# Optimization experiments

Measured on AMD Instinct MI355X. Metric: run time of the kernel, lower is better.

The kernel has to match this reference:

```python
import jax, jax.numpy as jnp
import numpy as np

D_MODEL = 1024
NUM_HEADS = 16
HEAD_DIM = D_MODEL // NUM_HEADS
D_FF = 4 * D_MODEL


def setup_inputs() -> dict:
    key = jax.random.key(0)
    ks = jax.random.split(key, 16)
    s = 0.02
    inp = {
        "x": jax.random.normal(ks[0], (2, 2048, D_MODEL), dtype=jnp.float32),
        "w_q": jax.random.normal(ks[1], (D_MODEL, D_MODEL), dtype=jnp.float32) * s,
        "b_q": jnp.zeros((D_MODEL,), jnp.float32),
        "w_k": jax.random.normal(ks[2], (D_MODEL, D_MODEL), dtype=jnp.float32) * s,
        "b_k": jnp.zeros((D_MODEL,), jnp.float32),
        "w_v": jax.random.normal(ks[3], (D_MODEL, D_MODEL), dtype=jnp.float32) * s,
        "b_v": jnp.zeros((D_MODEL,), jnp.float32),
        "w_o": jax.random.normal(ks[4], (D_MODEL, D_MODEL), dtype=jnp.float32) * s,
        "b_o": jnp.zeros((D_MODEL,), jnp.float32),
        "w_ff1": jax.random.normal(ks[5], (D_MODEL, D_FF), dtype=jnp.float32) * s,
        "b_ff1": jnp.zeros((D_FF,), jnp.float32),
        "w_ff2": jax.random.normal(ks[6], (D_FF, D_MODEL), dtype=jnp.float32) * s,
        "b_ff2": jnp.zeros((D_MODEL,), jnp.float32),
        "ln1_g": jnp.ones((D_MODEL,), jnp.float32),
        "ln1_b": jnp.zeros((D_MODEL,), jnp.float32),
        "ln2_g": jnp.ones((D_MODEL,), jnp.float32),
        "ln2_b": jnp.zeros((D_MODEL,), jnp.float32),
    }
    return inp


def layer_norm(x, g, b, eps=1e-5):
    mu = jnp.mean(x, axis=-1, keepdims=True)
    var = jnp.var(x, axis=-1, keepdims=True)
    return (x - mu) * jax.lax.rsqrt(var + eps) * g + b


def encoder_block(x, w_q, b_q, w_k, b_k, w_v, b_v, w_o, b_o,
                  w_ff1, b_ff1, w_ff2, b_ff2, ln1_g, ln1_b, ln2_g, ln2_b):
    B, S, _ = x.shape
    # QKV projections -> [B, H, S, hd]
    def proj(w, b):
        return (x @ w + b).reshape(B, S, NUM_HEADS, HEAD_DIM).transpose(0, 2, 1, 3)
    q, k, v = proj(w_q, b_q), proj(w_k, b_k), proj(w_v, b_v)
    scale = 1.0 / jnp.sqrt(jnp.float32(HEAD_DIM))
    score = jnp.einsum('bhqd,bhkd->bhqk', q, k) * scale  # [B,H,S,S]
    attn = jax.nn.softmax(score, axis=-1)
    ctx = jnp.einsum('bhqk,bhkd->bhqd', attn, v)
    ctx = ctx.transpose(0, 2, 1, 3).reshape(B, S, D_MODEL)
    attn_out = ctx @ w_o + b_o
    # AddNorm1 (dropout = identity at inference)
    h = layer_norm(x + attn_out, ln1_g, ln1_b)
    # FFN
    ff = jax.nn.relu(h @ w_ff1 + b_ff1) @ w_ff2 + b_ff2
    # AddNorm2
    return layer_norm(h + ff, ln2_g, ln2_b)


def reference(x, w_q, b_q, w_k, b_k, w_v, b_v, w_o, b_o,
              w_ff1, b_ff1, w_ff2, b_ff2, ln1_g, ln1_b, ln2_g, ln2_b):
    return encoder_block(x, w_q, b_q, w_k, b_k, w_v, b_v, w_o, b_o,
                         w_ff1, b_ff1, w_ff2, b_ff2, ln1_g, ln1_b, ln2_g, ln2_b)
```

## Files before the change

kernel.cpp:

```cpp
#include <hip/hip_runtime.h>
#include <hip/hip_bf16.h>

typedef __attribute__((ext_vector_type(8))) short short8;
typedef __attribute__((ext_vector_type(4))) float f32x4;
typedef unsigned short u16;
typedef unsigned int u32;

constexpr float CSC = 0.18033688f;

__device__ __forceinline__ u16 f2bf(float f) {
    __hip_bfloat16 h = __float2bfloat16(f);
    return __builtin_bit_cast(u16, h);
}
__device__ __forceinline__ u32 packtrunc(float a, float b) {
    const u32 ua = __builtin_bit_cast(u32, a);
    const u32 ub = __builtin_bit_cast(u32, b);
    return (ua >> 16) | (ub & 0xffff0000u);
}

#if __has_builtin(__builtin_amdgcn_exp2f)
#define EXP2(x) __builtin_amdgcn_exp2f(x)
#else
#define EXP2(x) exp2f(x)
#endif

#define GLD16(g, l) __builtin_amdgcn_global_load_lds( \
    (const __attribute__((address_space(1))) void*)(g), \
    (__attribute__((address_space(3))) void*)(l), 16, 0, 0)

__global__ __launch_bounds__(256) void prep_kernel(
    const float* __restrict__ x, u16* __restrict__ xb,
    const float* __restrict__ w_q, const float* __restrict__ w_k,
    const float* __restrict__ w_v, const float* __restrict__ w_o,
    const float* __restrict__ w_ff1, const float* __restrict__ w_ff2,
    u16* __restrict__ wqkvT, u16* __restrict__ woT,
    u16* __restrict__ wf1T, u16* __restrict__ wf2T,
    const float* __restrict__ bq, const float* __restrict__ bk,
    const float* __restrict__ bv, float* __restrict__ bout)
{
    __shared__ float tile[32][33];
    int id = blockIdx.x;
    const int t = threadIdx.x;
    if (id < 1024) {
        const int i = id * 256 + t;
        float4 v = ((const float4*)x)[i];
        *(ushort4*)(xb + 4 * (size_t)i) =
            make_ushort4(f2bf(v.x), f2bf(v.y), f2bf(v.z), f2bf(v.w));
        return;
    }
    id -= 1024;
    const float* src; u16* dst; int R, C, bx, by;
    if (id < 4096) {
        const int w = id >> 10, tt = id & 1023;
        src = w == 0 ? w_q : (w == 1 ? w_k : (w == 2 ? w_v : w_o));
        dst = w < 3 ? wqkvT + (size_t)w * 1024 * 1024 : woT;
        R = 1024; C = 1024; bx = (tt & 31) * 32; by = (tt >> 5) * 32;
    } else if (id < 8192) {
        const int tt = id - 4096;
        src = w_ff1; dst = wf1T;
        R = 1024; C = 4096; bx = (tt & 127) * 32; by = (tt >> 7) * 32;
    } else if (id < 12288) {
        const int tt = id - 8192;
        src = w_ff2; dst = wf2T;
        R = 4096; C = 1024; bx = (tt & 31) * 32; by = (tt >> 5) * 32;
    } else {
        for (int i = t; i < 1024; i += 256) {
            bout[i] = bq[i]; bout[1024 + i] = bk[i]; bout[2048 + i] = bv[i];
        }
        return;
    }
    const int tx = t & 31, ty = t >> 5;
    #pragma unroll
    for (int i = 0; i < 32; i += 8)
        tile[ty + i][tx] = src[(size_t)(by + ty + i) * C + bx + tx];
    __syncthreads();
    #pragma unroll
    for (int i = 0; i < 32; i += 8)
        dst[(size_t)(bx + ty + i) * R + by + tx] = f2bf(tile[tx][ty + i]);
}

template<bool RELU, int TM, bool QKV>
__global__ __launch_bounds__(256, 3) void gemm_bt(
    const u16* __restrict__ A, const u16* __restrict__ BT,
    const float* __restrict__ bias, u16* __restrict__ C,
    u16* __restrict__ VT, int M, int N, int K)
{
    __shared__ __align__(16) u16 As[TM * 32];
    __shared__ __align__(16) u16 Bs[128 * 32];
    constexpr int MW = TM / 32;
    constexpr int NCH_A = TM * 4;
    constexpr int NITER = (NCH_A + 512) / 256;
    const int t = threadIdx.x;
    const int wave = t >> 6, lane = t & 63;
    const int quad = lane >> 4, l16 = lane & 15;
    const int wm = (wave >> 1) * (TM / 2), wn = (wave & 1) * 64;
    const size_t rowA = (size_t)blockIdx.x * TM;
    const size_t rowB = (size_t)blockIdx.y * 128;

    f32x4 acc[MW][4] = {};

    for (int k0 = 0; k0 < K; k0 += 32) {
        __syncthreads();
        #pragma unroll
        for (int j = 0; j < NITER; ++j) {
            const int cb = j * 256 + wave * 64;
            const int c = cb + lane;
            if (j * 256 < NCH_A) {
                const int m = c >> 2, kq = c & 3;
                GLD16(A + (rowA + m) * K + k0 + kq * 8, As + cb * 8);
            } else {
                const int c2 = c - NCH_A;
                const int m = c2 >> 2, kq = c2 & 3;
                GLD16(BT + (rowB + m) * K + k0 + kq * 8, Bs + (cb - NCH_A) * 8);
            }
        }
        __syncthreads();
        short8 af[MW], bf[4];
        #pragma unroll
        for (int i = 0; i < MW; ++i)
            af[i] = *(const short8*)(As + (wm + i * 16 + l16) * 32 + quad * 8);
        #pragma unroll
        for (int j = 0; j < 4; ++j)
            bf[j] = *(const short8*)(Bs + (wn + j * 16 + l16) * 32 + quad * 8);
        #pragma unroll
        for (int i = 0; i < MW; ++i)
            #pragma unroll
            for (int j = 0; j < 4; ++j)
                acc[i][j] = __builtin_amdgcn_mfma_f32_16x16x32_bf16(
                    af[i], bf[j], acc[i][j], 0, 0, 0);
    }

    if (QKV && (int)blockIdx.y >= 16) {
        #pragma unroll
        for (int i = 0; i < MW; ++i) {
            #pragma unroll
            for (int j = 0; j < 4; ++j) {
                const int vcol = (int)rowB + wn + j * 16 + l16 - 2048;
                const int hh = vcol >> 6, dd = vcol & 63;
                const float bv = bias[vcol + 2048];
                const int row0 = (int)rowA + wm + i * 16 + quad * 4;
                const int bb = row0 >> 11, ss = row0 & 2047;
                ushort4 pk;
                pk.x = f2bf(acc[i][j][0] + bv);
                pk.y = f2bf(acc[i][j][1] + bv);
                pk.z = f2bf(acc[i][j][2] + bv);
                pk.w = f2bf(acc[i][j][3] + bv);
                *(ushort4*)(VT + ((size_t)(bb * 16 + hh) * 64 + dd) * 2048 + ss) = pk;
            }
        }
    } else {
        const float sc = (QKV && (int)blockIdx.y < 8) ? CSC : 1.0f;
        #pragma unroll
        for (int i = 0; i < MW; ++i) {
            #pragma unroll
            for (int j = 0; j < 4; ++j) {
                const int col = (int)rowB + wn + j * 16 + l16;
                const float bv = bias[col];
                #pragma unroll
                for (int r = 0; r < 4; ++r) {
                    const int row = (int)rowA + wm + i * 16 + quad * 4 + r;
                    float v = (acc[i][j][r] + bv) * sc;
                    if (RELU) v = fmaxf(v, 0.f);
                    C[(size_t)row * N + col] = f2bf(v);
                }
            }
        }
    }
}

template<int TM>
__global__ __launch_bounds__(256, 3) void gemm_bt_sk(
    const u16* __restrict__ A, const u16* __restrict__ BT,
    float* __restrict__ Cp0, float* __restrict__ Cp1,
    int M, int N, int K, int Kspl)
{
    __shared__ __align__(16) u16 As[TM * 32];
    __shared__ __align__(16) u16 Bs[128 * 32];
    constexpr int MW = TM / 32;
    constexpr int NCH_A = TM * 4;
    constexpr int NITER = (NCH_A + 512) / 256;
    const int t = threadIdx.x;
    const int wave = t >> 6, lane = t & 63;
    const int quad = lane >> 4, l16 = lane & 15;
    const int wm = (wave >> 1) * (TM / 2), wn = (wave & 1) * 64;
    const size_t rowA = (size_t)blockIdx.x * TM;
    const size_t rowB = (size_t)blockIdx.y * 128;
    const int kbeg = blockIdx.z * Kspl;

    f32x4 acc[MW][4] = {};

    for (int k0 = kbeg; k0 < kbeg + Kspl; k0 += 32) {
        __syncthreads();
        #pragma unroll
        for (int j = 0; j < NITER; ++j) {
            const int cb = j * 256 + wave * 64;
            const int c = cb + lane;
            if (j * 256 < NCH_A) {
                const int m = c >> 2, kq = c & 3;
                GLD16(A + (rowA + m) * K + k0 + kq * 8, As + cb * 8);
            } else {
                const int c2 = c - NCH_A;
                const int m = c2 >> 2, kq = c2 & 3;
                GLD16(BT + (rowB + m) * K + k0 + kq * 8, Bs + (cb - NCH_A) * 8);
            }
        }
        __syncthreads();
        short8 af[MW], bf[4];
        #pragma unroll
        for (int i = 0; i < MW; ++i)
            af[i] = *(const short8*)(As + (wm + i * 16 + l16) * 32 + quad * 8);
        #pragma unroll
        for (int j = 0; j < 4; ++j)
            bf[j] = *(const short8*)(Bs + (wn + j * 16 + l16) * 32 + quad * 8);
        #pragma unroll
        for (int i = 0; i < MW; ++i)
            #pragma unroll
            for (int j = 0; j < 4; ++j)
                acc[i][j] = __builtin_amdgcn_mfma_f32_16x16x32_bf16(
                    af[i], bf[j], acc[i][j], 0, 0, 0);
    }

    float* out = blockIdx.z == 0 ? Cp0 : Cp1;
    #pragma unroll
    for (int i = 0; i < MW; ++i)
        #pragma unroll
        for (int j = 0; j < 4; ++j) {
            const int col = (int)rowB + wn + j * 16 + l16;
            #pragma unroll
            for (int r = 0; r < 4; ++r) {
                const int row = (int)rowA + wm + i * 16 + quad * 4 + r;
                out[(size_t)row * N + col] = acc[i][j][r];
            }
        }
}

__global__ __launch_bounds__(256, 2) void flash_attn(
    const u16* __restrict__ qkv, const u16* __restrict__ vt,
    u16* __restrict__ ctx)
{
    __shared__ __align__(16) u16 Ks[64 * 64];
    __shared__ __align__(16) u16 Vs[64 * 64];
    __shared__ __align__(16) u16 Ps[4 * 32 * 72];
    const int t = threadIdx.x;
    const int wave = t >> 6, lane = t & 63;
    const int quad = lane >> 4, l16 = lane & 15;
    const int h = blockIdx.y, b = blockIdx.z;
    const int q0 = blockIdx.x * 128 + wave * 32;
    const size_t rowbase = (size_t)b * 2048;
    const u16* kb = qkv + rowbase * 3072 + 1024 + h * 64;
    const u16* vb = vt + (size_t)(b * 16 + h) * 64 * 2048;
    u16* pw = Ps + wave * 32 * 72;

    short8 aq[2][2];
    #pragma unroll
    for (int m2 = 0; m2 < 2; ++m2)
        #pragma unroll
        for (int ksb = 0; ksb < 2; ++ksb)
            aq[m2][ksb] = *(const short8*)(qkv +
                (rowbase + q0 + m2 * 16 + l16) * 3072 + h * 64 + ksb * 32 + quad * 8);

    f32x4 o[2][4] = {};
    f32x4 lp4[2] = {};

    for (int kv0 = 0; kv0 < 2048; kv0 += 64) {
        __syncthreads();
        #pragma unroll
        for (int j = 0; j < 2; ++j) {
            const int cb = j * 256 + wave * 64;
            const int slot = cb + lane;
            const int row = slot >> 3;
            const int kq = (slot & 7) ^ (row & 7);
            GLD16(kb + (size_t)(kv0 + row) * 3072 + kq * 8, Ks + cb * 8);
            GLD16(vb + (size_t)row * 2048 + kv0 + kq * 8, Vs + cb * 8);
        }
        __syncthreads();

        f32x4 st[2][4] = {};
        #pragma unroll
        for (int ksb = 0; ksb < 2; ++ksb) {
            short8 ak[4];
            #pragma unroll
            for (int mt = 0; mt < 4; ++mt)
                ak[mt] = *(const short8*)(Ks +
                    ((mt * 16 + l16) * 8 + ((ksb * 4 + quad) ^ (l16 & 7))) * 8);
            #pragma unroll
            for (int m2 = 0; m2 < 2; ++m2)
                #pragma unroll
                for (int mt = 0; mt < 4; ++mt)
                    st[m2][mt] = __builtin_amdgcn_mfma_f32_16x16x32_bf16(
                        ak[mt], aq[m2][ksb], st[m2][mt], 0, 0, 0);
        }

        #pragma unroll
        for (int m2 = 0; m2 < 2; ++m2) {
            #pragma unroll
            for (int mt = 0; mt < 4; ++mt) {
                const float p0 = EXP2(st[m2][mt][0]);
                const float p1 = EXP2(st[m2][mt][1]);
                const float p2 = EXP2(st[m2][mt][2]);
                const float p3 = EXP2(st[m2][mt][3]);
                lp4[m2] = lp4[m2] + (f32x4){p0, p1, p2, p3};
                *(uint2*)(pw + (m2 * 16 + l16) * 72 + mt * 16 + quad * 4) =
                    make_uint2(packtrunc(p0, p1), packtrunc(p2, p3));
            }
        }

        #pragma unroll
        for (int ksb = 0; ksb < 2; ++ksb) {
            short8 bv[4];
            #pragma unroll
            for (int dt = 0; dt < 4; ++dt)
                bv[dt] = *(const short8*)(Vs +
                    ((dt * 16 + l16) * 8 + ((ksb * 4 + quad) ^ (l16 & 7))) * 8);
            #pragma unroll
            for (int m2 = 0; m2 < 2; ++m2) {
                const short8 ap = *(const short8*)(pw +
                    (m2 * 16 + l16) * 72 + ksb * 32 + quad * 8);
                #pragma unroll
                for (int dt = 0; dt < 4; ++dt)
                    o[m2][dt] = __builtin_amdgcn_mfma_f32_16x16x32_bf16(
                        ap, bv[dt], o[m2][dt], 0, 0, 0);
            }
        }
    }

    #pragma unroll
    for (int m2 = 0; m2 < 2; ++m2) {
        float lp = (lp4[m2][0] + lp4[m2][1]) + (lp4[m2][2] + lp4[m2][3]);
        lp += __shfl_xor(lp, 16, 64);
        lp += __shfl_xor(lp, 32, 64);
        #pragma unroll
        for (int r = 0; r < 4; ++r) {
            const float inv = 1.0f / __shfl(lp, quad * 4 + r, 64);
            const size_t row = rowbase + q0 + m2 * 16 + quad * 4 + r;
            #pragma unroll
            for (int dt = 0; dt < 4; ++dt)
                ctx[row * 1024 + h * 64 + dt * 16 + l16] = f2bf(o[m2][dt][r] * inv);
        }
    }
}

__global__ __launch_bounds__(256) void add_norm_p_kernel(
    const float* __restrict__ a, const float* __restrict__ p0,
    const float* __restrict__ p1, const float* __restrict__ cb,
    const float* __restrict__ g, const float* __restrict__ bbv,
    float* __restrict__ out32, u16* __restrict__ out16)
{
    __shared__ float red[8];
    const int row = blockIdx.x, t = threadIdx.x;
    const int wave = t >> 6, lane = t & 63;
    const size_t base = (size_t)row * 1024 + t * 4;
    const int c = t * 4;
    float4 av = *(const float4*)(a + base);
    float4 q0 = *(const float4*)(p0 + base);
    float4 q1 = *(const float4*)(p1 + base);
    float4 cv = *(const float4*)(cb + c);
    float v0 = av.x + q0.x + q1.x + cv.x;
    float v1 = av.y + q0.y + q1.y + cv.y;
    float v2 = av.z + q0.z + q1.z + cv.z;
    float v3 = av.w + q0.w + q1.w + cv.w;
    float sum = v0 + v1 + v2 + v3;
    float sq  = v0 * v0 + v1 * v1 + v2 * v2 + v3 * v3;
    #pragma unroll
    for (int msk = 1; msk < 64; msk <<= 1) {
        sum += __shfl_xor(sum, msk, 64);
        sq  += __shfl_xor(sq,  msk, 64);
    }
    if (lane == 0) { red[wave] = sum; red[wave + 4] = sq; }
    __syncthreads();
    sum = red[0] + red[1] + red[2] + red[3];
    sq  = red[4] + red[5] + red[6] + red[7];
    const float mu  = sum * (1.f / 1024.f);
    const float var = sq * (1.f / 1024.f) - mu * mu;
    const float rstd = rsqrtf(var + 1e-5f);
    float o0 = (v0 - mu) * rstd * g[c + 0] + bbv[c + 0];
    float o1 = (v1 - mu) * rstd * g[c + 1] + bbv[c + 1];
    float o2 = (v2 - mu) * rstd * g[c + 2] + bbv[c + 2];
    float o3 = (v3 - mu) * rstd * g[c + 3] + bbv[c + 3];
    *(float4*)(out32 + base) = make_float4(o0, o1, o2, o3);
    if (out16)
        *(ushort4*)(out16 + base) = make_ushort4(f2bf(o0), f2bf(o1), f2bf(o2), f2bf(o3));
}

extern "C" void kernel_launch(void* const* d_in, const int* in_sizes, int n_in,
                              void* d_out, int out_size, void* d_ws, size_t ws_size,
                              hipStream_t stream)
{
    const float* x     = (const float*)d_in[0];
    const float* w_q   = (const float*)d_in[1];
    const float* b_q   = (const float*)d_in[2];
    const float* w_k   = (const float*)d_in[3];
    const float* b_k   = (const float*)d_in[4];
    const float* w_v   = (const float*)d_in[5];
    const float* b_v   = (const float*)d_in[6];
    const float* w_o   = (const float*)d_in[7];
    const float* b_o   = (const float*)d_in[8];
    const float* w_ff1 = (const float*)d_in[9];
    const float* b_ff1 = (const float*)d_in[10];
    const float* w_ff2 = (const float*)d_in[11];
    const float* b_ff2 = (const float*)d_in[12];
    const float* ln1_g = (const float*)d_in[13];
    const float* ln1_b = (const float*)d_in[14];
    const float* ln2_g = (const float*)d_in[15];
    const float* ln2_b = (const float*)d_in[16];

    char* ws = (char*)d_ws;
    u16*   xb    = (u16*)(ws);
    u16*   wqkvT = (u16*)(ws + (8ull  << 20));
    u16*   woT   = (u16*)(ws + (14ull << 20));
    u16*   wf1T  = (u16*)(ws + (16ull << 20));
    u16*   wf2T  = (u16*)(ws + (24ull << 20));
    float* bqkv  = (float*)(ws + (32ull << 20));
    u16*   qkv   = (u16*)(ws + (33ull << 20));
    u16*   ctx   = (u16*)(ws + (57ull << 20));
    float* h32   = (float*)(ws + (65ull << 20));
    u16*   hb    = (u16*)(ws + (81ull << 20));
    u16*   ff    = (u16*)(ws + (89ull << 20));
    u16*   vt    = (u16*)(ws + (121ull << 20));
    float* pO0   = (float*)(ws + (33ull << 20));
    float* pO1   = (float*)(ws + (121ull << 20));
    float* pF0   = (float*)(ws + (33ull << 20));
    float* pF1   = (float*)(ws + (49ull << 20));

    prep_kernel<<<13313, 256, 0, stream>>>(
        x, xb, w_q, w_k, w_v, w_o, w_ff1, w_ff2,
        wqkvT, woT, wf1T, wf2T, b_q, b_k, b_v, bqkv);

    gemm_bt<false, 128, true ><<<dim3(32, 24), 256, 0, stream>>>(
        xb, wqkvT, bqkv, qkv, vt, 4096, 3072, 1024);
    flash_attn<<<dim3(16, 16, 2), 256, 0, stream>>>(qkv, vt, ctx);
    gemm_bt_sk<128><<<dim3(32, 8, 2), 256, 0, stream>>>(
        ctx, woT, pO0, pO1, 4096, 1024, 1024, 512);
    add_norm_p_kernel<<<4096, 256, 0, stream>>>(
        x, pO0, pO1, b_o, ln1_g, ln1_b, h32, hb);
    gemm_bt<true, 128, false><<<dim3(32, 32), 256, 0, stream>>>(
        hb, wf1T, b_ff1, ff, nullptr, 4096, 4096, 1024);
    gemm_bt_sk<128><<<dim3(32, 8, 2), 256, 0, stream>>>(
        ff, wf2T, pF0, pF1, 4096, 1024, 4096, 2048);
    add_norm_p_kernel<<<4096, 256, 0, stream>>>(
        h32, pF0, pF1, b_ff2, ln2_g, ln2_b, (float*)d_out, nullptr);
}
```

Baseline: 349.2 us.

## Store split-K partials as bf16 and shrink split-K GEMM tiles to 64 rows

The split-K GEMMs for the output projection and FFN2 now write their partial sums as bf16 instead of fp32, and the add-norm kernel reads and converts them, halving partial-buffer traffic. The split-K tile height drops from 128 to 64 with twice the grid in M, and launch bounds ask for 4 blocks per CU, for more parallelism. Rounding each partial to bf16 before the residual add loses accuracy, and the smaller tiles reduce operand reuse.

After: 345.9 us. No clear change (-0.9%).

```diff
diff --git a/kernel.cpp b/kernel.cpp
--- a/kernel.cpp
+++ b/kernel.cpp
@@ -11,6 +11,10 @@
 __device__ __forceinline__ u16 f2bf(float f) {
     __hip_bfloat16 h = __float2bfloat16(f);
     return __builtin_bit_cast(u16, h);
+}
+__device__ __forceinline__ float bf2f(u16 u) {
+    __hip_bfloat16 h = __builtin_bit_cast(__hip_bfloat16, u);
+    return __bfloat162float(h);
 }
 __device__ __forceinline__ u32 packtrunc(float a, float b) {
     const u32 ua = __builtin_bit_cast(u32, a);
@@ -169,9 +173,9 @@
 }
 
 template<int TM>
-__global__ __launch_bounds__(256, 3) void gemm_bt_sk(
+__global__ __launch_bounds__(256, 4) void gemm_bt_sk(
     const u16* __restrict__ A, const u16* __restrict__ BT,
-    float* __restrict__ Cp0, float* __restrict__ Cp1,
+    u16* __restrict__ Cp0, u16* __restrict__ Cp1,
     int M, int N, int K, int Kspl)
 {
     __shared__ __align__(16) u16 As[TM * 32];
@@ -220,7 +224,7 @@
                     af[i], bf[j], acc[i][j], 0, 0, 0);
     }
 
-    float* out = blockIdx.z == 0 ? Cp0 : Cp1;
+    u16* out = blockIdx.z == 0 ? Cp0 : Cp1;
     #pragma unroll
     for (int i = 0; i < MW; ++i)
         #pragma unroll
@@ -229,7 +233,7 @@
             #pragma unroll
             for (int r = 0; r < 4; ++r) {
                 const int row = (int)rowA + wm + i * 16 + quad * 4 + r;
-                out[(size_t)row * N + col] = acc[i][j][r];
+                out[(size_t)row * N + col] = f2bf(acc[i][j][r]);
             }
         }
 }
@@ -341,8 +345,8 @@
 }
 
 __global__ __launch_bounds__(256) void add_norm_p_kernel(
-    const float* __restrict__ a, const float* __restrict__ p0,
-    const float* __restrict__ p1, const float* __restrict__ cb,
+    const float* __restrict__ a, const u16* __restrict__ p0,
+    const u16* __restrict__ p1, const float* __restrict__ cb,
     const float* __restrict__ g, const float* __restrict__ bbv,
     float* __restrict__ out32, u16* __restrict__ out16)
 {
@@ -352,13 +356,13 @@
     const size_t base = (size_t)row * 1024 + t * 4;
     const int c = t * 4;
     float4 av = *(const float4*)(a + base);
-    float4 q0 = *(const float4*)(p0 + base);
-    float4 q1 = *(const float4*)(p1 + base);
+    ushort4 u0 = *(const ushort4*)(p0 + base);
+    ushort4 u1 = *(const ushort4*)(p1 + base);
     float4 cv = *(const float4*)(cb + c);
-    float v0 = av.x + q0.x + q1.x + cv.x;
-    float v1 = av.y + q0.y + q1.y + cv.y;
-    float v2 = av.z + q0.z + q1.z + cv.z;
-    float v3 = av.w + q0.w + q1.w + cv.w;
+    float v0 = av.x + bf2f(u0.x) + bf2f(u1.x) + cv.x;
+    float v1 = av.y + bf2f(u0.y) + bf2f(u1.y) + cv.y;
+    float v2 = av.z + bf2f(u0.z) + bf2f(u1.z) + cv.z;
+    float v3 = av.w + bf2f(u0.w) + bf2f(u1.w) + cv.w;
     float sum = v0 + v1 + v2 + v3;
     float sq  = v0 * v0 + v1 * v1 + v2 * v2 + v3 * v3;
     #pragma unroll
@@ -417,10 +421,10 @@
     u16*   hb    = (u16*)(ws + (81ull << 20));
     u16*   ff    = (u16*)(ws + (89ull << 20));
     u16*   vt    = (u16*)(ws + (121ull << 20));
-    float* pO0   = (float*)(ws + (33ull << 20));
-    float* pO1   = (float*)(ws + (121ull << 20));
-    float* pF0   = (float*)(ws + (33ull << 20));
-    float* pF1   = (float*)(ws + (49ull << 20));
+    u16*   pO0   = (u16*)(ws + (33ull << 20));
+    u16*   pO1   = (u16*)(ws + (41ull << 20));
+    u16*   pF0   = (u16*)(ws + (33ull << 20));
+    u16*   pF1   = (u16*)(ws + (41ull << 20));
 
     prep_kernel<<<13313, 256, 0, stream>>>(
         x, xb, w_q, w_k, w_v, w_o, w_ff1, w_ff2,
@@ -429,13 +433,13 @@
     gemm_bt<false, 128, true ><<<dim3(32, 24), 256, 0, stream>>>(
         xb, wqkvT, bqkv, qkv, vt, 4096, 3072, 1024);
     flash_attn<<<dim3(16, 16, 2), 256, 0, stream>>>(qkv, vt, ctx);
-    gemm_bt_sk<128><<<dim3(32, 8, 2), 256, 0, stream>>>(
+    gemm_bt_sk<64><<<dim3(64, 8, 2), 256, 0, stream>>>(
         ctx, woT, pO0, pO1, 4096, 1024, 1024, 512);
     add_norm_p_kernel<<<4096, 256, 0, stream>>>(
         x, pO0, pO1, b_o, ln1_g, ln1_b, h32, hb);
     gemm_bt<true, 128, false><<<dim3(32, 32), 256, 0, stream>>>(
         hb, wf1T, b_ff1, ff, nullptr, 4096, 4096, 1024);
-    gemm_bt_sk<128><<<dim3(32, 8, 2), 256, 0, stream>>>(
+    gemm_bt_sk<64><<<dim3(64, 8, 2), 256, 0, stream>>>(
         ff, wf2T, pF0, pF1, 4096, 1024, 4096, 2048);
     add_norm_p_kernel<<<4096, 256, 0, stream>>>(
         h32, pF0, pF1, b_ff2, ln2_g, ln2_b, (float*)d_out, nullptr);
```
